# Optimization experiments

Hardware: AMD Instinct MI355X
Metric: run time of the kernel (lower is better)

## Reference

```python
import jax, jax.numpy as jnp
import numpy as np

KS = 3
N = KS ** 3  # 27 kernel taps
EPS = 1e-5

def conv3d(x, w, stride=1, padding=0):
    return jax.lax.conv_general_dilated(
        x, w, (stride,) * 3, [(padding, padding)] * 3,
        dimension_numbers=('NCDHW', 'OIDHW', 'NCDHW'))

def batchnorm(x, gamma, beta):
    mu = jnp.mean(x, axis=(0, 2, 3, 4), keepdims=True)
    var = jnp.var(x, axis=(0, 2, 3, 4), keepdims=True)
    return (x - mu) * jax.lax.rsqrt(var + EPS) * gamma[None, :, None, None, None] + beta[None, :, None, None, None]

def deform_conv3d(x, w_p, b_p, w_m, b_m, w_dc):
    b, c, D, H, W = x.shape
    offset = conv3d(x, w_p, padding=1) + b_p[None, :, None, None, None]      # (b,3N,D,H,W)
    m = jax.nn.sigmoid(conv3d(x, w_m, padding=1) + b_m[None, :, None, None, None])  # (b,N,D,H,W)
    x_pad = jnp.pad(x, ((0, 0), (0, 0), (1, 1), (1, 1), (1, 1)))
    Dp, Hp, Wp = D + 2, H + 2, W + 2
    r = jnp.arange(-(KS - 1) // 2, KS // 2 + 1, dtype=x.dtype)
    pn_d, pn_h, pn_w = [a.reshape(-1) for a in jnp.meshgrid(r, r, r, indexing='ij')]
    off = offset.transpose(0, 2, 3, 4, 1)                                    # (b,D,H,W,3N)
    p0_d = jnp.arange(1, D + 1, dtype=x.dtype)[:, None, None, None]
    p0_h = jnp.arange(1, H + 1, dtype=x.dtype)[None, :, None, None]
    p0_w = jnp.arange(1, W + 1, dtype=x.dtype)[None, None, :, None]
    pd = p0_d + pn_d + off[..., :N]
    ph = p0_h + pn_h + off[..., N:2 * N]
    pw = p0_w + pn_w + off[..., 2 * N:]
    d0 = jnp.clip(jnp.floor(pd), 0.0, Dp - 1.0); d1 = jnp.clip(d0 + 1.0, 0.0, Dp - 1.0)
    h0 = jnp.clip(jnp.floor(ph), 0.0, Hp - 1.0); h1 = jnp.clip(h0 + 1.0, 0.0, Hp - 1.0)
    w0 = jnp.clip(jnp.floor(pw), 0.0, Wp - 1.0); w1 = jnp.clip(w0 + 1.0, 0.0, Wp - 1.0)
    pd = jnp.clip(pd, 0.0, Dp - 1.0); ph = jnp.clip(ph, 0.0, Hp - 1.0); pw = jnp.clip(pw, 0.0, Wp - 1.0)
    xf = x_pad.reshape(b, c, -1)
    def gather(qd, qh, qw):
        idx = (qd * (Hp * Wp) + qh * Wp + qw).astype(jnp.int32).reshape(b, 1, -1)
        v = jnp.take_along_axis(xf, jnp.broadcast_to(idx, (b, c, idx.shape[-1])), axis=2)
        return v.reshape(b, c, D, H, W, N)
    x_off = jnp.zeros((b, c, D, H, W, N), x.dtype)
    for qd, wd in ((d0, 1.0 + d0 - pd), (d1, 1.0 - d1 + pd)):
        for qh, wh in ((h0, 1.0 + h0 - ph), (h1, 1.0 - h1 + ph)):
            for qw, ww in ((w0, 1.0 + w0 - pw), (w1, 1.0 - w1 + pw)):
                x_off = x_off + (wd * wh * ww)[:, None] * gather(qd, qh, qw)
    x_off = x_off * m.transpose(0, 2, 3, 4, 1)[:, None]                      # modulation
    # interleave kernel taps: (b,c,D,kd,H,kh,W,kw) -> (b,c,D*KS,H*KS,W*KS)
    x_off = x_off.reshape(b, c, D, H, W, KS, KS, KS)
    x_off = x_off.transpose(0, 1, 2, 5, 3, 6, 4, 7).reshape(b, c, D * KS, H * KS, W * KS)
    out = conv3d(x_off, w_dc, stride=KS)
    p = jnp.concatenate([pd, ph, pw], axis=-1)                               # (b,D,H,W,3N)
    return out, p

def setup_inputs() -> dict:
    key = jax.random.key(0)
    ks = jax.random.split(key, 10)
    B, D = 4, 48
    return {
        'x': jax.random.normal(ks[0], (B, 1, D, D, D), jnp.float32),
        'w_p': jax.random.normal(ks[1], (3 * N, 1, KS, KS, KS), jnp.float32) * 0.05,
        'b_p': jnp.zeros((3 * N,), jnp.float32),
        'w_m': jax.random.normal(ks[2], (N, 1, KS, KS, KS), jnp.float32) * 0.1,
        'b_m': jnp.zeros((N,), jnp.float32),
        'w_dc': jax.random.normal(ks[3], (1, 1, KS, KS, KS), jnp.float32) * 0.2,
        'g_d': jnp.ones((1,), jnp.float32), 'be_d': jnp.zeros((1,), jnp.float32),
        'w_c1': jax.random.normal(ks[4], (32, 1, KS, KS, KS), jnp.float32) * 0.3,
        'g1': jnp.ones((32,), jnp.float32), 'be1': jnp.zeros((32,), jnp.float32),
        'w_c2': jax.random.normal(ks[5], (64, 32, KS, KS, KS), jnp.float32) * 0.06,
        'g2': jnp.ones((64,), jnp.float32), 'be2': jnp.zeros((64,), jnp.float32),
        'w_fc': jax.random.normal(ks[6], (10, 64), jnp.float32) * 0.1,
        'b_fc': jnp.zeros((10,), jnp.float32),
    }

def reference(x, w_p, b_p, w_m, b_m, w_dc, g_d, be_d, w_c1, g1, be1, w_c2, g2, be2, w_fc, b_fc):
    inp = x
    for _ in range(2):
        y, p = deform_conv3d(inp, w_p, b_p, w_m, b_m, w_dc)
        xxx = y
        inp = jax.nn.relu(batchnorm(y, g_d, be_d))
    h = jax.nn.relu(batchnorm(conv3d(inp, w_c1, padding=1), g1, be1))
    h = jax.nn.relu(batchnorm(conv3d(h, w_c2, padding=1), g2, be2))
    h = jax.lax.reduce_window(h, -jnp.inf, jax.lax.max, (1, 1, 3, 3, 3), (1, 1, 3, 3, 3), 'VALID')
    h = h.mean(axis=(2, 3, 4))                       # adaptive avg pool to 1
    logits = h @ w_fc.T + b_fc
    return logits, xxx, p
```

## Files before the change

kernel.cpp:

```cpp
#include <hip/hip_runtime.h>
#include <math.h>

#define BSZ 4
#define DD 48
#define SS (48*48*48)
#define NV (BSZ*SS)
#define PS 125000
#define EPSBN 1e-5f

typedef __attribute__((ext_vector_type(8))) short bf16x8;
typedef __attribute__((ext_vector_type(4))) short s16x4;
typedef __attribute__((ext_vector_type(4))) float f32x4;

__device__ __forceinline__ short f2b(float f){
  unsigned u = __float_as_uint(f);
  u = (u + 0x7FFFu + ((u>>16)&1u)) >> 16;
  return (short)u;
}
__device__ __forceinline__ float b2f(short s){
  return __uint_as_float(((unsigned)(unsigned short)s)<<16);
}

__global__ __launch_bounds__(256) void pad_pair_kernel(
    const float* __restrict__ src, unsigned* __restrict__ dst)
{
  int idx = blockIdx.x*256 + threadIdx.x;
  if (idx >= BSZ*PS) return;
  int b = idx / PS; int r = idx - b*PS;
  int z = r/2500; int r2 = r - z*2500; int yy = r2/50; int xx = r2 - yy*50;
  const float* sb = src + (size_t)b*SS;
  auto val = [&](int zz,int yv,int xv)->unsigned{
    float v = 0.f;
    if (zz>=1 && zz<=48 && yv>=1 && yv<=48 && xv>=1 && xv<=48)
      v = sb[(size_t)((zz-1)*48 + (yv-1))*48 + (xv-1)];
    return (unsigned)(unsigned short)f2b(v);
  };
  unsigned lo = val(z,yy,xx);
  unsigned hi = (xx<49) ? val(z,yy,xx+1) : 0u;
  dst[idx] = lo | (hi<<16);
}

__global__ __launch_bounds__(256) void bnpad_pair_kernel(
    const float* __restrict__ y, const float* __restrict__ st,
    const float* __restrict__ gamma, const float* __restrict__ beta,
    unsigned* __restrict__ dst)
{
  int idx = blockIdx.x*256 + threadIdx.x;
  if (idx >= BSZ*PS) return;
  float mu  = st[0]*(1.f/(float)NV);
  float var = st[1]*(1.f/(float)NV) - mu*mu;
  float sc  = rsqrtf(var+EPSBN)*gamma[0];
  float sh  = beta[0] - mu*sc;
  int b = idx / PS; int r = idx - b*PS;
  int z = r/2500; int r2 = r - z*2500; int yy = r2/50; int xx = r2 - yy*50;
  const float* yb = y + (size_t)b*SS;
  auto val = [&](int zz,int yv,int xv)->unsigned{
    float v = 0.f;
    if (zz>=1 && zz<=48 && yv>=1 && yv<=48 && xv>=1 && xv<=48){
      float t = yb[(size_t)((zz-1)*48 + (yv-1))*48 + (xv-1)];
      v = fmaxf(fmaf(t, sc, sh), 0.f);
    }
    return (unsigned)(unsigned short)f2b(v);
  };
  unsigned lo = val(z,yy,xx);
  unsigned hi = (xx<49) ? val(z,yy,xx+1) : 0u;
  dst[idx] = lo | (hi<<16);
}

__global__ void woff2_kernel(const float* __restrict__ w_p, const float* __restrict__ b_p,
                             const float* __restrict__ w_m, const float* __restrict__ b_m,
                             short* __restrict__ wo2)
{
  int o = blockIdx.x*256 + threadIdx.x;
  if (o >= 112*32) return;
  int k = o & 31; int c = o >> 5;
  int f = c >> 4, qq = (c >> 2) & 3, r = c & 3;
  int n = 4*f + qq;
  float v = 0.f;
  if (n < 27){
    if (k < 27)       v = (r < 3) ? w_p[(r*27+n)*27 + k] : w_m[n*27 + k];
    else if (k == 27) v = (r < 3) ? b_p[r*27+n]          : b_m[n];
  }
  wo2[o] = f2b(v);
}

__global__ void wconv1_kernel(const float* __restrict__ w, short* __restrict__ wb)
{
  int o = blockIdx.x*256 + threadIdx.x;
  if (o >= 32*32) return;
  int k = o & 31; int c = o >> 5;
  wb[o] = f2b(k < 27 ? w[c*27 + k] : 0.f);
}

template<bool WRITE_P>
__global__ __launch_bounds__(256) void deform3_kernel(
    const unsigned* __restrict__ xpair,
    const short* __restrict__ wo2,
    const float* __restrict__ w_dc,
    float* __restrict__ y, float* __restrict__ p_out,
    float* __restrict__ st)
{
  __shared__ short xt[6*6*18];
  __shared__ __align__(16) float pbuf[WRITE_P ? 4*16*81 : 4];
  __shared__ float yred[8];

  int bid = blockIdx.x;
  int bw = bid % 3; int bh = (bid/3)%12; int bd = (bid/36)%12; int b = bid/432;
  int d0 = bd*4, h0 = bh*4, w0 = bw*16;
  int tid = threadIdx.x;
  const unsigned* xp = xpair + (size_t)b*PS;

  for (int e = tid; e < 648; e += 256){
    int z = e/108; int rem = e - z*108; int yy = rem/18; int xx = rem - yy*18;
    xt[e] = (short)(xp[(d0+z)*2500 + (h0+yy)*50 + (w0+xx)] & 0xffffu);
  }
  __syncthreads();

  int lane = tid & 63, wid = tid >> 6;
  int q = lane >> 4, n16 = lane & 15;

  bf16x8 aF[7];
  #pragma unroll
  for (int f=0; f<7; ++f)
    aF[f] = *(const bf16x8*)(wo2 + (f*16 + n16)*32 + q*8);

  int toffs[8];
  #pragma unroll
  for (int j=0;j<8;++j){
    int t = q*8 + j; int tc = t > 26 ? 0 : t;
    int kd = tc/9, rr = tc - kd*9, kh = rr/3, kw = rr - kh*3;
    toffs[j] = kd*108 + kh*18 + kw;
  }

  float wdcv[7], fkd[7], fkh[7], fkw[7];
  #pragma unroll
  for (int f=0; f<7; ++f){
    int n = 4*f + q;
    if (n < 27){
      int kd = n/9, rr = n - kd*9, kh = rr/3, kw = rr - kh*3;
      wdcv[f] = w_dc[n];
      fkd[f] = (float)kd; fkh[f] = (float)kh; fkw[f] = (float)kw;
    } else { wdcv[f]=0.f; fkd[f]=0.f; fkh[f]=0.f; fkw[f]=0.f; }
  }

  const short one_bf = (short)0x3F80;
  const f32x4 zero4 = {0.f,0.f,0.f,0.f};
  float based = (float)(d0 + wid);
  float basew = (float)(w0 + n16);
  float ys = 0.f, yq = 0.f;
  float* pw = pbuf + wid*1296;

  #pragma unroll 1
  for (int dy=0; dy<4; ++dy){
    int vbase = wid*108 + dy*18 + n16;
    bf16x8 bF;
    #pragma unroll
    for (int j=0;j<8;++j){
      short xv = xt[vbase + toffs[j]];
      bF[j] = (j<3 || q<3) ? xv : one_bf;
    }
    f32x4 acc[7];
    #pragma unroll
    for (int f=0; f<7; ++f)
      acc[f] = __builtin_amdgcn_mfma_f32_16x16x32_bf16(aF[f], bF, zero4, 0,0,0);

    float baseh = (float)(h0 + dy);
    float accv = 0.f;
    #pragma unroll
    for (int f=0; f<7; ++f){
      int n = 4*f + q;
      if (n < 27){
        float od = acc[f][0], oh = acc[f][1], ow = acc[f][2], mr = acc[f][3];
        float mm = __builtin_amdgcn_rcpf(1.f + __expf(-mr));
        float pdv = based + fkd[f] + od;
        float phv = baseh + fkh[f] + oh;
        float pwv = basew + fkw[f] + ow;
        float fd0 = fminf(fmaxf(floorf(pdv),0.f),49.f), fd1 = fminf(fd0+1.f,49.f);
        float pdc = fminf(fmaxf(pdv,0.f),49.f);
        float wd0 = 1.f + fd0 - pdc, wd1 = 1.f - fd1 + pdc;
        float fh0 = fminf(fmaxf(floorf(phv),0.f),49.f), fh1 = fminf(fh0+1.f,49.f);
        float phc = fminf(fmaxf(phv,0.f),49.f);
        float wh0 = 1.f + fh0 - phc, wh1 = 1.f - fh1 + phc;
        float fw0 = fminf(fmaxf(floorf(pwv),0.f),49.f);
        float pwc = fminf(fmaxf(pwv,0.f),49.f);
        float fw1 = fminf(fw0+1.f,49.f);
        float wwa = 1.f + fw0 - pwc, wwb = 1.f - fw1 + pwc;
        int iz0 = (int)fd0*2500, iz1 = (int)fd1*2500;
        int iy0 = (int)fh0*50,   iy1 = (int)fh1*50;
        int ix0 = (int)fw0;
        bool sel = ix0 > 48;
        int ixp = sel ? 48 : ix0;
        unsigned p00 = xp[iz0+iy0+ixp], p01 = xp[iz0+iy1+ixp];
        unsigned p10 = xp[iz1+iy0+ixp], p11 = xp[iz1+iy1+ixp];
        float lo00=b2f((short)p00), hi00=b2f((short)(p00>>16));
        float lo01=b2f((short)p01), hi01=b2f((short)(p01>>16));
        float lo10=b2f((short)p10), hi10=b2f((short)(p10>>16));
        float lo11=b2f((short)p11), hi11=b2f((short)(p11>>16));
        float v000 = sel ? hi00 : lo00, v001 = hi00;
        float v010 = sel ? hi01 : lo01, v011 = hi01;
        float v100 = sel ? hi10 : lo10, v101 = hi10;
        float v110 = sel ? hi11 : lo11, v111 = hi11;
        float sv = wd0*(wh0*(wwa*v000+wwb*v001)+wh1*(wwa*v010+wwb*v011))
                 + wd1*(wh0*(wwa*v100+wwb*v101)+wh1*(wwa*v110+wwb*v111));
        accv += sv*mm*wdcv[f];
        if constexpr (WRITE_P){
          int vb = n16*81;
          pw[vb + n]      = pdc;
          pw[vb + 27 + n] = phc;
          pw[vb + 54 + n] = pwc;
        }
      }
    }
    accv += __shfl_xor(accv, 16);
    accv += __shfl_xor(accv, 32);
    if (q == 0){
      y[(size_t)b*SS + (size_t)((d0+wid)*48 + (h0+dy))*48 + (w0+n16)] = accv;
      ys += accv; yq += accv*accv;
    }

    if constexpr (WRITE_P){
      size_t rbase = ((((size_t)b*48 + (d0+wid))*48 + (h0+dy))*48 + w0)*81;
      float* dst = p_out + rbase;
      #pragma unroll
      for (int k=0;k<6;++k){
        int i = lane + (k<<6);
        if (i < 324){
          f32x4 v = *(const f32x4*)(pw + i*4);
          *(f32x4*)(dst + i*4) = v;
        }
      }
    }
  }

  ys += __shfl_xor(ys, 1); ys += __shfl_xor(ys, 2);
  ys += __shfl_xor(ys, 4); ys += __shfl_xor(ys, 8);
  yq += __shfl_xor(yq, 1); yq += __shfl_xor(yq, 2);
  yq += __shfl_xor(yq, 4); yq += __shfl_xor(yq, 8);
  if (lane == 0){ yred[wid] = ys; yred[4+wid] = yq; }
  __syncthreads();
  if (tid == 0) atomicAdd(&st[0], yred[0]+yred[1]+yred[2]+yred[3]);
  if (tid == 1) atomicAdd(&st[1], yred[4]+yred[5]+yred[6]+yred[7]);
}

__global__ __launch_bounds__(256) void conv1m_kernel(
    const unsigned* __restrict__ xpair, const short* __restrict__ wc1b,
    short* __restrict__ h1c)
{
  __shared__ short xt[6*6*18];
  int bid = blockIdx.x;
  int bw = bid % 3; int bh = (bid/3)%12; int bd = (bid/36)%12; int b = bid/432;
  int d0 = bd*4, h0 = bh*4, w0 = bw*16;
  int tid = threadIdx.x;
  const unsigned* xp = xpair + (size_t)b*PS;

  for (int e = tid; e < 648; e += 256){
    int z = e/108; int rem = e - z*108; int yy = rem/18; int xx = rem - yy*18;
    xt[e] = (short)(xp[(d0+z)*2500 + (h0+yy)*50 + (w0+xx)] & 0xffffu);
  }
  __syncthreads();

  int lane = tid & 63, wid = tid >> 6;
  int q = lane >> 4, n16 = lane & 15;

  bf16x8 aF0 = *(const bf16x8*)(wc1b + n16*32 + q*8);
  bf16x8 aF1 = *(const bf16x8*)(wc1b + (16+n16)*32 + q*8);

  int toffs[8];
  #pragma unroll
  for (int j=0;j<8;++j){
    int t = q*8 + j; int tc = t > 26 ? 0 : t;
    int kd = tc/9, rr = tc - kd*9, kh = rr/3, kw = rr - kh*3;
    toffs[j] = kd*108 + kh*18 + kw;
  }

  const f32x4 zero4 = {0.f,0.f,0.f,0.f};
  #pragma unroll
  for (int dy=0; dy<4; ++dy){
    int vbase = wid*108 + dy*18 + n16;
    bf16x8 bF;
    #pragma unroll
    for (int j=0;j<8;++j) bF[j] = xt[vbase + toffs[j]];
    f32x4 a0 = __builtin_amdgcn_mfma_f32_16x16x32_bf16(aF0, bF, zero4, 0,0,0);
    f32x4 a1 = __builtin_amdgcn_mfma_f32_16x16x32_bf16(aF1, bF, zero4, 0,0,0);
    size_t idx = (size_t)b*SS + (size_t)((d0+wid)*48 + (h0+dy))*48 + (w0+n16);
    s16x4 o0, o1;
    #pragma unroll
    for (int r=0;r<4;++r){ o0[r]=f2b(a0[r]); o1[r]=f2b(a1[r]); }
    *(s16x4*)(h1c + idx*32 + q*4)      = o0;
    *(s16x4*)(h1c + idx*32 + 16 + q*4) = o1;
  }
}

template<int NCH>
__global__ __launch_bounds__(256) void bn_stats_cl(
    const short* __restrict__ x, float* __restrict__ sums)
{
  constexpr int GPB = NCH/8;
  const long NG = (long)NV*GPB;
  int tid = threadIdx.x;
  f32x4 sa = {0.f,0.f,0.f,0.f}, sb = sa, qa = sa, qb = sa;
  for (long g = (long)blockIdx.x*256+tid; g < NG; g += (long)gridDim.x*256){
    bf16x8 v8 = *(const bf16x8*)(x + g*8);
    float v;
    v=b2f(v8[0]); sa[0]+=v; qa[0]+=v*v;
    v=b2f(v8[1]); sa[1]+=v; qa[1]+=v*v;
    v=b2f(v8[2]); sa[2]+=v; qa[2]+=v*v;
    v=b2f(v8[3]); sa[3]+=v; qa[3]+=v*v;
    v=b2f(v8[4]); sb[0]+=v; qb[0]+=v*v;
    v=b2f(v8[5]); sb[1]+=v; qb[1]+=v*v;
    v=b2f(v8[6]); sb[2]+=v; qb[2]+=v*v;
    v=b2f(v8[7]); sb[3]+=v; qb[3]+=v*v;
  }
  #pragma unroll
  for (int m = GPB; m < 64; m <<= 1){
    sa[0]+=__shfl_xor(sa[0],m); sa[1]+=__shfl_xor(sa[1],m);
    sa[2]+=__shfl_xor(sa[2],m); sa[3]+=__shfl_xor(sa[3],m);
    sb[0]+=__shfl_xor(sb[0],m); sb[1]+=__shfl_xor(sb[1],m);
    sb[2]+=__shfl_xor(sb[2],m); sb[3]+=__shfl_xor(sb[3],m);
    qa[0]+=__shfl_xor(qa[0],m); qa[1]+=__shfl_xor(qa[1],m);
    qa[2]+=__shfl_xor(qa[2],m); qa[3]+=__shfl_xor(qa[3],m);
    qb[0]+=__shfl_xor(qb[0],m); qb[1]+=__shfl_xor(qb[1],m);
    qb[2]+=__shfl_xor(qb[2],m); qb[3]+=__shfl_xor(qb[3],m);
  }
  int lane = tid & 63, wid = tid >> 6;
  __shared__ float red[4][GPB][16];
  if (lane < GPB){
    red[wid][lane][0]=sa[0];  red[wid][lane][1]=sa[1];
    red[wid][lane][2]=sa[2];  red[wid][lane][3]=sa[3];
    red[wid][lane][4]=sb[0];  red[wid][lane][5]=sb[1];
    red[wid][lane][6]=sb[2];  red[wid][lane][7]=sb[3];
    red[wid][lane][8]=qa[0];  red[wid][lane][9]=qa[1];
    red[wid][lane][10]=qa[2]; red[wid][lane][11]=qa[3];
    red[wid][lane][12]=qb[0]; red[wid][lane][13]=qb[1];
    red[wid][lane][14]=qb[2]; red[wid][lane][15]=qb[3];
  }
  __syncthreads();
  if (tid < GPB*16){
    int gi = tid >> 4, v = tid & 15;
    float t = red[0][gi][v] + red[1][gi][v] + red[2][gi][v] + red[3][gi][v];
    int ch = gi*8 + (v & 7);
    atomicAdd(&sums[2*ch + (v>>3)], t);
  }
}

__global__ __launch_bounds__(256) void conv2_mfma2(
    const short* __restrict__ h1c, const short* __restrict__ wbf,
    const float* __restrict__ st1, const float* __restrict__ g1,
    const float* __restrict__ be1, short* __restrict__ t2c)
{
  __shared__ __align__(16) short slab[4*648*8];
  __shared__ float ssc[32], ssh[32];
  int tid = threadIdx.x;
  if (tid < 32){
    float mu  = st1[2*tid]  *(1.f/(float)NV);
    float var = st1[2*tid+1]*(1.f/(float)NV) - mu*mu;
    float sc = rsqrtf(var+EPSBN)*g1[tid];
    ssc[tid]=sc; ssh[tid]=be1[tid]-mu*sc;
  }
  __syncthreads();

  int bid0 = blockIdx.x;
  int bid = (bid0 & 7)*216 + (bid0 >> 3);
  int bw = bid % 3; int bh = (bid/3)%12; int bd = (bid/36)%12; int b = bid/432;
  int d0 = bd*4, h0 = bh*4, w0 = bw*16;
  const short* hb = h1c + (size_t)b*SS*32;

  for (int e = tid; e < 648; e += 256){
    int z = e/108; int rem = e - z*108; int y = rem/18; int x = rem - y*18;
    int gd = d0-1+z, gh = h0-1+y, gw = w0-1+x;
    bool ok = ((unsigned)gd<48u)&&((unsigned)gh<48u)&&((unsigned)gw<48u);
    if (ok){
      const bf16x8* src = (const bf16x8*)(hb + (size_t)((gd*48+gh)*48+gw)*32);
      #pragma unroll
      for (int g8=0; g8<4; ++g8){
        bf16x8 raw = src[g8];
        bf16x8 outv;
        #pragma unroll
        for (int j=0;j<8;++j){
          float v = fmaxf(fmaf(b2f(raw[j]), ssc[g8*8+j], ssh[g8*8+j]), 0.f);
          outv[j] = f2b(v);
        }
        *(bf16x8*)&slab[(g8*648+e)*8] = outv;
      }
    } else {
      bf16x8 zz = {0,0,0,0,0,0,0,0};
      #pragma unroll
      for (int g8=0; g8<4; ++g8) *(bf16x8*)&slab[(g8*648+e)*8] = zz;
    }
  }
  __syncthreads();

  int lane = tid & 63, wid = tid >> 6;
  int q = lane >> 4, n16 = lane & 15;
  f32x4 zero4 = {0.f,0.f,0.f,0.f};
  f32x4 acc[4][4];
  #pragma unroll
  for (int i=0;i<4;++i)
  #pragma unroll
  for (int j=0;j<4;++j) acc[i][j] = zero4;

  #pragma unroll 1
  for (int tap=0; tap<27; ++tap){
    int kd = tap/9; int kh = (tap/3)%3; int kw = tap%3;
    const short* wp = wbf + (size_t)tap*64*32 + n16*32 + q*8;
    bf16x8 aF[4];
    #pragma unroll
    for (int mb=0; mb<4; ++mb)
      aF[mb] = *(const bf16x8*)(wp + mb*16*32);

    int zz = wid + kd;
    #pragma unroll
    for (int dy=0; dy<4; ++dy){
      int e = (zz*6 + (dy+kh))*18 + (n16+kw);
      bf16x8 bF = *(const bf16x8*)&slab[(q*648 + e)*8];
      #pragma unroll
      for (int mb=0; mb<4; ++mb)
        acc[mb][dy] = __builtin_amdgcn_mfma_f32_16x16x32_bf16(aF[mb], bF, acc[mb][dy], 0,0,0);
    }
  }

  short* tb = t2c + (size_t)b*SS*64;
  #pragma unroll
  for (int dy=0; dy<4; ++dy){
    int svox = ((d0+wid)*48 + (h0+dy))*48 + (w0+n16);
    #pragma unroll
    for (int mb=0; mb<4; ++mb){
      s16x4 o4;
      #pragma unroll
      for (int r=0;r<4;++r) o4[r] = f2b(acc[mb][dy][r]);
      *(s16x4*)(tb + (size_t)svox*64 + mb*16 + q*4) = o4;
    }
  }
}

__global__ void wconv_kernel(const float* __restrict__ w, short* __restrict__ wbf)
{
  int o = blockIdx.x*blockDim.x + threadIdx.x;
  if (o >= 27*64*32) return;
  int ci = o & 31; int co = (o>>5) & 63; int tap = o >> 11;
  wbf[o] = f2b(w[(co*32+ci)*27 + tap]);
}

__global__ __launch_bounds__(128) void pool64c_kernel(
    const short* __restrict__ t2c, const float* __restrict__ sums,
    const float* __restrict__ gamma, const float* __restrict__ beta,
    float* __restrict__ pooled)
{
  __shared__ float ssc[64], ssh[64];
  int tid = threadIdx.x;
  if (tid < 64){
    float mu  = sums[2*tid]  *(1.f/(float)NV);
    float var = sums[2*tid+1]*(1.f/(float)NV) - mu*mu;
    float sc = rsqrtf(var+EPSBN)*gamma[tid];
    ssc[tid]=sc; ssh[tid]=beta[tid]-mu*sc;
  }
  __syncthreads();
  int b = blockIdx.z, pd = blockIdx.y, ph = blockIdx.x;
  int c8 = tid & 7, pw = tid >> 3;
  const short* tb = t2c + (size_t)b*SS*64;
  f32x4 mxa = {-1e30f,-1e30f,-1e30f,-1e30f}, mxb = mxa;
  float sc0=ssc[c8*8+0], sc1=ssc[c8*8+1], sc2=ssc[c8*8+2], sc3=ssc[c8*8+3];
  float sc4=ssc[c8*8+4], sc5=ssc[c8*8+5], sc6=ssc[c8*8+6], sc7=ssc[c8*8+7];
  float sh0=ssh[c8*8+0], sh1=ssh[c8*8+1], sh2=ssh[c8*8+2], sh3=ssh[c8*8+3];
  float sh4=ssh[c8*8+4], sh5=ssh[c8*8+5], sh6=ssh[c8*8+6], sh7=ssh[c8*8+7];
  #pragma unroll
  for (int kd=0;kd<3;++kd)
  #pragma unroll 1
  for (int kh=0;kh<3;++kh)
  #pragma unroll
  for (int kw=0;kw<3;++kw){
    int vox = ((pd*3+kd)*48 + (ph*3+kh))*48 + (pw*3+kw);
    bf16x8 v8 = *(const bf16x8*)(tb + (size_t)vox*64 + c8*8);
    float v;
    v = fmaxf(fmaf(b2f(v8[0]), sc0, sh0), 0.f); mxa[0] = fmaxf(mxa[0], v);
    v = fmaxf(fmaf(b2f(v8[1]), sc1, sh1), 0.f); mxa[1] = fmaxf(mxa[1], v);
    v = fmaxf(fmaf(b2f(v8[2]), sc2, sh2), 0.f); mxa[2] = fmaxf(mxa[2], v);
    v = fmaxf(fmaf(b2f(v8[3]), sc3, sh3), 0.f); mxa[3] = fmaxf(mxa[3], v);
    v = fmaxf(fmaf(b2f(v8[4]), sc4, sh4), 0.f); mxb[0] = fmaxf(mxb[0], v);
    v = fmaxf(fmaf(b2f(v8[5]), sc5, sh5), 0.f); mxb[1] = fmaxf(mxb[1], v);
    v = fmaxf(fmaf(b2f(v8[6]), sc6, sh6), 0.f); mxb[2] = fmaxf(mxb[2], v);
    v = fmaxf(fmaf(b2f(v8[7]), sc7, sh7), 0.f); mxb[3] = fmaxf(mxb[3], v);
  }
  __shared__ float r[128][8];
  r[tid][0]=mxa[0]; r[tid][1]=mxa[1]; r[tid][2]=mxa[2]; r[tid][3]=mxa[3];
  r[tid][4]=mxb[0]; r[tid][5]=mxb[1]; r[tid][6]=mxb[2]; r[tid][7]=mxb[3];
  __syncthreads();
  for (int o=64;o>=8;o>>=1){
    if (tid<o){
      #pragma unroll
      for (int j=0;j<8;++j) r[tid][j]+=r[tid+o][j];
    }
    __syncthreads();
  }
  if (tid<8){
    #pragma unroll
    for (int j=0;j<8;++j) atomicAdd(&pooled[b*64 + tid*8 + j], r[tid][j]);
  }
}

__global__ void fc_kernel(const float* __restrict__ pooled,
                          const float* __restrict__ w_fc, const float* __restrict__ b_fc,
                          float* __restrict__ logits)
{
  int t = threadIdx.x;
  if (t < 40){
    int b = t/10, k = t - 10*(t/10);
    float a = b_fc[k];
    #pragma unroll 1
    for (int c=0;c<64;++c) a = fmaf(pooled[b*64+c]*(1.f/4096.f), w_fc[k*64+c], a);
    logits[b*10+k] = a;
  }
}

extern "C" void kernel_launch(void* const* d_in, const int* in_sizes, int n_in,
                              void* d_out, int out_size, void* d_ws, size_t ws_size,
                              hipStream_t stream)
{
  const float* x    = (const float*)d_in[0];
  const float* w_p  = (const float*)d_in[1];
  const float* b_p  = (const float*)d_in[2];
  const float* w_m  = (const float*)d_in[3];
  const float* b_m  = (const float*)d_in[4];
  const float* w_dc = (const float*)d_in[5];
  const float* g_d  = (const float*)d_in[6];
  const float* be_d = (const float*)d_in[7];
  const float* w_c1 = (const float*)d_in[8];
  const float* g1   = (const float*)d_in[9];
  const float* be1  = (const float*)d_in[10];
  const float* w_c2 = (const float*)d_in[11];
  const float* g2   = (const float*)d_in[12];
  const float* be2  = (const float*)d_in[13];
  const float* w_fc = (const float*)d_in[14];
  const float* b_fc = (const float*)d_in[15];

  float* out    = (float*)d_out;
  float* logits = out;
  float* xxx    = out + 40;
  float* p_out  = out + 40 + NV;

  float* ws     = (float*)d_ws;
  float* stats  = ws;
  float* pooled = stats + 512;
  short* wbf    = (short*)(pooled + 256);
  short* wo2    = wbf + 27*64*32;
  short* wc1b   = wo2 + 112*32;
  unsigned* xpair = (unsigned*)(wc1b + 32*32);
  float* y1     = (float*)(xpair + (size_t)BSZ*PS);
  short* h1c    = (short*)(y1 + NV);
  short* t2c    = h1c + (size_t)NV*32;

  float* st_y1 = stats + 0;
  float* st_y2 = stats + 2;
  float* st_h1 = stats + 4;
  float* st_t2 = stats + 68;

  const int pblk = (BSZ*PS + 255)/256;

  hipMemsetAsync(stats, 0, (512+256)*sizeof(float), stream);

  wconv_kernel<<<(27*64*32+255)/256,256,0,stream>>>(w_c2, wbf);
  woff2_kernel<<<(112*32+255)/256,256,0,stream>>>(w_p, b_p, w_m, b_m, wo2);
  wconv1_kernel<<<(32*32+255)/256,256,0,stream>>>(w_c1, wc1b);

  pad_pair_kernel<<<pblk,256,0,stream>>>(x, xpair);
  deform3_kernel<false><<<1728,256,0,stream>>>(xpair, wo2, w_dc, y1, nullptr, st_y1);
  bnpad_pair_kernel<<<pblk,256,0,stream>>>(y1, st_y1, g_d, be_d, xpair);

  deform3_kernel<true><<<1728,256,0,stream>>>(xpair, wo2, w_dc, xxx, p_out, st_y2);
  bnpad_pair_kernel<<<pblk,256,0,stream>>>(xxx, st_y2, g_d, be_d, xpair);

  conv1m_kernel<<<1728,256,0,stream>>>(xpair, wc1b, h1c);
  bn_stats_cl<32><<<256,256,0,stream>>>(h1c, st_h1);

  conv2_mfma2<<<1728,256,0,stream>>>(h1c, wbf, st_h1, g1, be1, t2c);
  bn_stats_cl<64><<<512,256,0,stream>>>(t2c, st_t2);
  pool64c_kernel<<<dim3(16,16,BSZ),128,0,stream>>>(t2c, st_t2, g2, be2, pooled);

  fc_kernel<<<1,64,0,stream>>>(pooled, w_fc, b_fc, logits);
}
```

Measured before the change: 342.0 us.

## Fuse BN statistics into conv epilogues and merge weight repack kernels

Per-channel sum and sum-of-squares for the two BN layers are now accumulated in the epilogues of conv1 and conv2. Values are reduced with wave shuffles and shared memory, then added with atomics, which removes the separate bn_stats passes that re-read both bf16 activation tensors. The three small weight-repacking kernels are merged into a single launch. The trade-off is extra registers and shuffle work in the conv epilogues and more atomics per block.

```diff
diff --git a/kernel.cpp b/kernel.cpp
--- a/kernel.cpp
+++ b/kernel.cpp
@@ -67,29 +67,33 @@
   dst[idx] = lo | (hi<<16);
 }
 
-__global__ void woff2_kernel(const float* __restrict__ w_p, const float* __restrict__ b_p,
-                             const float* __restrict__ w_m, const float* __restrict__ b_m,
-                             short* __restrict__ wo2)
+__global__ void repack_kernel(
+    const float* __restrict__ w_c2,
+    const float* __restrict__ w_p, const float* __restrict__ b_p,
+    const float* __restrict__ w_m, const float* __restrict__ b_m,
+    const float* __restrict__ w_c1,
+    short* __restrict__ wbf, short* __restrict__ wo2, short* __restrict__ wc1b)
 {
   int o = blockIdx.x*256 + threadIdx.x;
-  if (o >= 112*32) return;
-  int k = o & 31; int c = o >> 5;
-  int f = c >> 4, qq = (c >> 2) & 3, r = c & 3;
-  int n = 4*f + qq;
-  float v = 0.f;
-  if (n < 27){
-    if (k < 27)       v = (r < 3) ? w_p[(r*27+n)*27 + k] : w_m[n*27 + k];
-    else if (k == 27) v = (r < 3) ? b_p[r*27+n]          : b_m[n];
-  }
-  wo2[o] = f2b(v);
-}
-
-__global__ void wconv1_kernel(const float* __restrict__ w, short* __restrict__ wb)
-{
-  int o = blockIdx.x*256 + threadIdx.x;
-  if (o >= 32*32) return;
-  int k = o & 31; int c = o >> 5;
-  wb[o] = f2b(k < 27 ? w[c*27 + k] : 0.f);
+  if (o < 27*64*32){
+    int ci = o & 31; int co = (o>>5) & 63; int tap = o >> 11;
+    wbf[o] = f2b(w_c2[(co*32+ci)*27 + tap]);
+  } else if (o < 27*64*32 + 112*32){
+    int o2 = o - 27*64*32;
+    int k = o2 & 31; int c = o2 >> 5;
+    int f = c >> 4, qq = (c >> 2) & 3, r = c & 3;
+    int n = 4*f + qq;
+    float v = 0.f;
+    if (n < 27){
+      if (k < 27)       v = (r < 3) ? w_p[(r*27+n)*27 + k] : w_m[n*27 + k];
+      else if (k == 27) v = (r < 3) ? b_p[r*27+n]          : b_m[n];
+    }
+    wo2[o2] = f2b(v);
+  } else if (o < 27*64*32 + 112*32 + 32*32){
+    int o3 = o - 27*64*32 - 112*32;
+    int k = o3 & 31; int c = o3 >> 5;
+    wc1b[o3] = f2b(k < 27 ? w_c1[c*27 + k] : 0.f);
+  }
 }
 
 template<bool WRITE_P>
@@ -244,9 +248,10 @@
 
 __global__ __launch_bounds__(256) void conv1m_kernel(
     const unsigned* __restrict__ xpair, const short* __restrict__ wc1b,
-    short* __restrict__ h1c)
+    short* __restrict__ h1c, float* __restrict__ st)
 {
   __shared__ short xt[6*6*18];
+  __shared__ float red[4][4][16];
   int bid = blockIdx.x;
   int bw = bid % 3; int bh = (bid/3)%12; int bd = (bid/36)%12; int b = bid/432;
   int d0 = bd*4, h0 = bh*4, w0 = bw*16;
@@ -274,6 +279,7 @@
   }
 
   const f32x4 zero4 = {0.f,0.f,0.f,0.f};
+  f32x4 s0 = zero4, q0v = zero4, s1 = zero4, q1v = zero4;
   #pragma unroll
   for (int dy=0; dy<4; ++dy){
     int vbase = wid*108 + dy*18 + n16;
@@ -288,68 +294,49 @@
     for (int r=0;r<4;++r){ o0[r]=f2b(a0[r]); o1[r]=f2b(a1[r]); }
     *(s16x4*)(h1c + idx*32 + q*4)      = o0;
     *(s16x4*)(h1c + idx*32 + 16 + q*4) = o1;
-  }
-}
-
-template<int NCH>
-__global__ __launch_bounds__(256) void bn_stats_cl(
-    const short* __restrict__ x, float* __restrict__ sums)
-{
-  constexpr int GPB = NCH/8;
-  const long NG = (long)NV*GPB;
-  int tid = threadIdx.x;
-  f32x4 sa = {0.f,0.f,0.f,0.f}, sb = sa, qa = sa, qb = sa;
-  for (long g = (long)blockIdx.x*256+tid; g < NG; g += (long)gridDim.x*256){
-    bf16x8 v8 = *(const bf16x8*)(x + g*8);
-    float v;
-    v=b2f(v8[0]); sa[0]+=v; qa[0]+=v*v;
-    v=b2f(v8[1]); sa[1]+=v; qa[1]+=v*v;
-    v=b2f(v8[2]); sa[2]+=v; qa[2]+=v*v;
-    v=b2f(v8[3]); sa[3]+=v; qa[3]+=v*v;
-    v=b2f(v8[4]); sb[0]+=v; qb[0]+=v*v;
-    v=b2f(v8[5]); sb[1]+=v; qb[1]+=v*v;
-    v=b2f(v8[6]); sb[2]+=v; qb[2]+=v*v;
-    v=b2f(v8[7]); sb[3]+=v; qb[3]+=v*v;
-  }
-  #pragma unroll
-  for (int m = GPB; m < 64; m <<= 1){
-    sa[0]+=__shfl_xor(sa[0],m); sa[1]+=__shfl_xor(sa[1],m);
-    sa[2]+=__shfl_xor(sa[2],m); sa[3]+=__shfl_xor(sa[3],m);
-    sb[0]+=__shfl_xor(sb[0],m); sb[1]+=__shfl_xor(sb[1],m);
-    sb[2]+=__shfl_xor(sb[2],m); sb[3]+=__shfl_xor(sb[3],m);
-    qa[0]+=__shfl_xor(qa[0],m); qa[1]+=__shfl_xor(qa[1],m);
-    qa[2]+=__shfl_xor(qa[2],m); qa[3]+=__shfl_xor(qa[3],m);
-    qb[0]+=__shfl_xor(qb[0],m); qb[1]+=__shfl_xor(qb[1],m);
-    qb[2]+=__shfl_xor(qb[2],m); qb[3]+=__shfl_xor(qb[3],m);
-  }
-  int lane = tid & 63, wid = tid >> 6;
-  __shared__ float red[4][GPB][16];
-  if (lane < GPB){
-    red[wid][lane][0]=sa[0];  red[wid][lane][1]=sa[1];
-    red[wid][lane][2]=sa[2];  red[wid][lane][3]=sa[3];
-    red[wid][lane][4]=sb[0];  red[wid][lane][5]=sb[1];
-    red[wid][lane][6]=sb[2];  red[wid][lane][7]=sb[3];
-    red[wid][lane][8]=qa[0];  red[wid][lane][9]=qa[1];
-    red[wid][lane][10]=qa[2]; red[wid][lane][11]=qa[3];
-    red[wid][lane][12]=qb[0]; red[wid][lane][13]=qb[1];
-    red[wid][lane][14]=qb[2]; red[wid][lane][15]=qb[3];
-  }
-  __syncthreads();
-  if (tid < GPB*16){
-    int gi = tid >> 4, v = tid & 15;
-    float t = red[0][gi][v] + red[1][gi][v] + red[2][gi][v] + red[3][gi][v];
-    int ch = gi*8 + (v & 7);
-    atomicAdd(&sums[2*ch + (v>>3)], t);
+    #pragma unroll
+    for (int r=0;r<4;++r){
+      float v0 = b2f(o0[r]); s0[r]+=v0; q0v[r]+=v0*v0;
+      float v1 = b2f(o1[r]); s1[r]+=v1; q1v[r]+=v1*v1;
+    }
+  }
+  #pragma unroll
+  for (int m=1; m<16; m<<=1){
+    #pragma unroll
+    for (int r=0;r<4;++r){
+      s0[r]+=__shfl_xor(s0[r],m);  q0v[r]+=__shfl_xor(q0v[r],m);
+      s1[r]+=__shfl_xor(s1[r],m);  q1v[r]+=__shfl_xor(q1v[r],m);
+    }
+  }
+  if (n16 == 0){
+    #pragma unroll
+    for (int r=0;r<4;++r){
+      red[wid][q][r]    = s0[r];
+      red[wid][q][4+r]  = s1[r];
+      red[wid][q][8+r]  = q0v[r];
+      red[wid][q][12+r] = q1v[r];
+    }
+  }
+  __syncthreads();
+  if (tid < 64){
+    int qq = tid >> 4, v = tid & 15;
+    float t = red[0][qq][v] + red[1][qq][v] + red[2][qq][v] + red[3][qq][v];
+    int r = v & 3;
+    int ch = ((v>>2)&1) ? (16 + qq*4 + r) : (qq*4 + r);
+    int issq = v >> 3;
+    atomicAdd(&st[2*ch + issq], t);
   }
 }
 
 __global__ __launch_bounds__(256) void conv2_mfma2(
     const short* __restrict__ h1c, const short* __restrict__ wbf,
     const float* __restrict__ st1, const float* __restrict__ g1,
-    const float* __restrict__ be1, short* __restrict__ t2c)
+    const float* __restrict__ be1, short* __restrict__ t2c,
+    float* __restrict__ st2)
 {
   __shared__ __align__(16) short slab[4*648*8];
   __shared__ float ssc[32], ssh[32];
+  __shared__ float red[4][4][4][8];
   int tid = threadIdx.x;
   if (tid < 32){
     float mu  = st1[2*tid]  *(1.f/(float)NV);
@@ -420,6 +407,9 @@
   }
 
   short* tb = t2c + (size_t)b*SS*64;
+  f32x4 sacc[4], qacc[4];
+  #pragma unroll
+  for (int mb=0; mb<4; ++mb){ sacc[mb]=zero4; qacc[mb]=zero4; }
   #pragma unroll
   for (int dy=0; dy<4; ++dy){
     int svox = ((d0+wid)*48 + (h0+dy))*48 + (w0+n16);
@@ -427,18 +417,43 @@
     for (int mb=0; mb<4; ++mb){
       s16x4 o4;
       #pragma unroll
-      for (int r=0;r<4;++r) o4[r] = f2b(acc[mb][dy][r]);
+      for (int r=0;r<4;++r){
+        o4[r] = f2b(acc[mb][dy][r]);
+        float v = b2f(o4[r]);
+        sacc[mb][r] += v; qacc[mb][r] += v*v;
+      }
       *(s16x4*)(tb + (size_t)svox*64 + mb*16 + q*4) = o4;
     }
   }
-}
-
-__global__ void wconv_kernel(const float* __restrict__ w, short* __restrict__ wbf)
-{
-  int o = blockIdx.x*blockDim.x + threadIdx.x;
-  if (o >= 27*64*32) return;
-  int ci = o & 31; int co = (o>>5) & 63; int tap = o >> 11;
-  wbf[o] = f2b(w[(co*32+ci)*27 + tap]);
+  #pragma unroll
+  for (int m=1; m<16; m<<=1){
+    #pragma unroll
+    for (int mb=0; mb<4; ++mb){
+      #pragma unroll
+      for (int r=0;r<4;++r){
+        sacc[mb][r]+=__shfl_xor(sacc[mb][r],m);
+        qacc[mb][r]+=__shfl_xor(qacc[mb][r],m);
+      }
+    }
+  }
+  if (n16 == 0){
+    #pragma unroll
+    for (int mb=0; mb<4; ++mb){
+      #pragma unroll
+      for (int r=0;r<4;++r){
+        red[wid][q][mb][r]   = sacc[mb][r];
+        red[wid][q][mb][4+r] = qacc[mb][r];
+      }
+    }
+  }
+  __syncthreads();
+  if (tid < 128){
+    int qq = (tid>>5)&3, mb = (tid>>3)&3, v = tid&7;
+    float t = red[0][qq][mb][v] + red[1][qq][mb][v] + red[2][qq][mb][v] + red[3][qq][mb][v];
+    int r = v & 3, issq = v >> 2;
+    int ch = mb*16 + qq*4 + r;
+    atomicAdd(&st2[2*ch + issq], t);
+  }
 }
 
 __global__ __launch_bounds__(128) void pool64c_kernel(
@@ -558,9 +573,8 @@
 
   hipMemsetAsync(stats, 0, (512+256)*sizeof(float), stream);
 
-  wconv_kernel<<<(27*64*32+255)/256,256,0,stream>>>(w_c2, wbf);
-  woff2_kernel<<<(112*32+255)/256,256,0,stream>>>(w_p, b_p, w_m, b_m, wo2);
-  wconv1_kernel<<<(32*32+255)/256,256,0,stream>>>(w_c1, wc1b);
+  repack_kernel<<<(27*64*32 + 112*32 + 32*32 + 255)/256,256,0,stream>>>(
+      w_c2, w_p, b_p, w_m, b_m, w_c1, wbf, wo2, wc1b);
 
   pad_pair_kernel<<<pblk,256,0,stream>>>(x, xpair);
   deform3_kernel<false><<<1728,256,0,stream>>>(xpair, wo2, w_dc, y1, nullptr, st_y1);
@@ -569,11 +583,9 @@
   deform3_kernel<true><<<1728,256,0,stream>>>(xpair, wo2, w_dc, xxx, p_out, st_y2);
   bnpad_pair_kernel<<<pblk,256,0,stream>>>(xxx, st_y2, g_d, be_d, xpair);
 
-  conv1m_kernel<<<1728,256,0,stream>>>(xpair, wc1b, h1c);
-  bn_stats_cl<32><<<256,256,0,stream>>>(h1c, st_h1);
-
-  conv2_mfma2<<<1728,256,0,stream>>>(h1c, wbf, st_h1, g1, be1, t2c);
-  bn_stats_cl<64><<<512,256,0,stream>>>(t2c, st_t2);
+  conv1m_kernel<<<1728,256,0,stream>>>(xpair, wc1b, h1c, st_h1);
+
+  conv2_mfma2<<<1728,256,0,stream>>>(h1c, wbf, st_h1, g1, be1, t2c, st_t2);
   pool64c_kernel<<<dim3(16,16,BSZ),128,0,stream>>>(t2c, st_t2, g2, be2, pooled);
 
   fc_kernel<<<1,64,0,stream>>>(pooled, w_fc, b_fc, logits);
```

After: 428.2 us. 25.2% more time.
